# Optimization experiments

Hardware: AMD Instinct MI355X
Metric: run time of the kernel (lower is better)

The kernel has to match this reference:

```python
import jax, jax.numpy as jnp
import numpy as np

N_NODES = 50000
N_EDGES = 800000
DIMS = [100, 512, 256, 128, 200]  # input -> conv1 -> conv2 -> conv3 -> conv4


def setup_inputs() -> dict:
    key = jax.random.key(0)
    ks = jax.random.split(key, 2 + 4)
    x = jax.random.normal(ks[0], (N_NODES, DIMS[0]), dtype=jnp.float32)
    edge_index = jax.random.randint(ks[1], (2, N_EDGES), 0, N_NODES, dtype=jnp.int64)
    inp = {"x": x, "edge_index": edge_index}
    for i in range(4):
        fan_in = DIMS[i]
        W = jax.random.normal(ks[2 + i], (DIMS[i], DIMS[i + 1]), dtype=jnp.float32) * (1.0 / np.sqrt(fan_in)).astype(np.float32)
        b = jnp.zeros((DIMS[i + 1],), dtype=jnp.float32)
        inp[f"W{i + 1}"] = W
        inp[f"b{i + 1}"] = b
    return inp


def _gcn_layer(x, row, col, norm, W, b, n):
    # PyG GCNConv: linear transform first, then normalized scatter-add, then bias.
    h = x @ W                           # [N, out]
    msg = h[row] * norm[:, None]        # [E+N, out] gather + edge scale
    agg = jax.ops.segment_sum(msg, col, num_segments=n)  # scatter-add to targets
    return agg + b


def reference(x, edge_index, W1, b1, W2, b2, W3, b3, W4, b4):
    n = x.shape[0]
    loop = jnp.arange(n, dtype=edge_index.dtype)
    row = jnp.concatenate([edge_index[0], loop])  # sources (with self-loops)
    col = jnp.concatenate([edge_index[1], loop])  # targets (with self-loops)
    deg = jax.ops.segment_sum(jnp.ones_like(col, dtype=x.dtype), col, num_segments=n)
    dinv = jnp.where(deg > 0, jax.lax.rsqrt(deg), 0.0)
    norm = dinv[row] * dinv[col]  # symmetric D^{-1/2}(A+I)D^{-1/2} edge weights

    out = jax.nn.relu(_gcn_layer(x, row, col, norm, W1, b1, n))
    out = jax.nn.relu(_gcn_layer(out, row, col, norm, W2, b2, n))
    out = jax.nn.relu(_gcn_layer(out, row, col, norm, W3, b3, n))
    out = jax.nn.relu(_gcn_layer(out, row, col, norm, W4, b4, n))
    return jnp.mean(out, axis=0, keepdims=True)  # [1, 200]
```

## Files before the change

### kernel.cpp

```cpp
#include <hip/hip_runtime.h>
#include <hip/hip_bf16.h>


#define NN 50000
#define NE 800000
#define NPART 8
#define PRANGE (NN / NPART)

typedef __attribute__((ext_vector_type(8))) _Float16 f16x8;
typedef __attribute__((ext_vector_type(4))) float floatx4;
typedef __attribute__((ext_vector_type(2))) float floatx2;

union U16x8 {
    uint4 u4;
    f16x8 h;
    _Float16 e[8];
};

__device__ __forceinline__ void dec16(const unsigned char* p, float* f) {
    uint4 v = *(const uint4*)p;
    unsigned w[4] = {v.x, v.y, v.z, v.w};
#pragma unroll
    for (int k = 0; k < 4; k++) {
        floatx2 lo = __builtin_amdgcn_cvt_pk_f32_fp8(w[k], false);
        floatx2 hi = __builtin_amdgcn_cvt_pk_f32_fp8(w[k], true);
        f[k * 4 + 0] = lo[0];
        f[k * 4 + 1] = lo[1];
        f[k * 4 + 2] = hi[0];
        f[k * 4 + 3] = hi[1];
    }
}

__device__ __forceinline__ uint4 enc16(const float* f) {
    uint4 r;
    unsigned w;
    w = __builtin_amdgcn_cvt_pk_fp8_f32(f[0], f[1], 0, false);
    w = __builtin_amdgcn_cvt_pk_fp8_f32(f[2], f[3], (int)w, true);
    r.x = w;
    w = __builtin_amdgcn_cvt_pk_fp8_f32(f[4], f[5], 0, false);
    w = __builtin_amdgcn_cvt_pk_fp8_f32(f[6], f[7], (int)w, true);
    r.y = w;
    w = __builtin_amdgcn_cvt_pk_fp8_f32(f[8], f[9], 0, false);
    w = __builtin_amdgcn_cvt_pk_fp8_f32(f[10], f[11], (int)w, true);
    r.z = w;
    w = __builtin_amdgcn_cvt_pk_fp8_f32(f[12], f[13], 0, false);
    w = __builtin_amdgcn_cvt_pk_fp8_f32(f[14], f[15], (int)w, true);
    r.w = w;
    return r;
}

__device__ __forceinline__ uint4 dec8_f16(uint2 v) {
    floatx2 f0 = __builtin_amdgcn_cvt_pk_f32_fp8(v.x, false);
    floatx2 f1 = __builtin_amdgcn_cvt_pk_f32_fp8(v.x, true);
    floatx2 f2 = __builtin_amdgcn_cvt_pk_f32_fp8(v.y, false);
    floatx2 f3 = __builtin_amdgcn_cvt_pk_f32_fp8(v.y, true);
    U16x8 o;
    o.e[0] = (_Float16)f0[0]; o.e[1] = (_Float16)f0[1];
    o.e[2] = (_Float16)f1[0]; o.e[3] = (_Float16)f1[1];
    o.e[4] = (_Float16)f2[0]; o.e[5] = (_Float16)f2[1];
    o.e[6] = (_Float16)f3[0]; o.e[7] = (_Float16)f3[1];
    return o.u4;
}

__global__ __launch_bounds__(256) void zero_detect_kernel(
    const unsigned* __restrict__ ei, int* __restrict__ flag,
    unsigned* __restrict__ cnt, unsigned* __restrict__ fillc,
    float* __restrict__ out) {
    int tid = blockIdx.x * 256 + threadIdx.x;
    if (tid < NN) {
        cnt[tid] = 0u;
        fillc[tid] = 0u;
    }
    if (blockIdx.x == 0) {
        if (threadIdx.x < 200) out[threadIdx.x] = 0.f;
        unsigned w = ei[2 * threadIdx.x + 1];
        unsigned long long any = __ballot(w != 0);
        if (threadIdx.x == 0) *flag = (any == 0ull) ? 1 : 0;
    }
}

__global__ __launch_bounds__(256) void count_kernel(const void* ei,
                                                    const int* __restrict__ flag,
                                                    unsigned* __restrict__ cnt) {
    const int part = blockIdx.x & 7;
    const int lo = part * PRANGE, hi = lo + PRANGE;
    const int group = blockIdx.x >> 3;
    const int f64 = *flag;
    const long long* p64 = (const long long*)ei + NE;
    const int* p32 = (const int*)ei + NE;
    for (int e = group * 256 + threadIdx.x; e < NE; e += 128 * 256) {
        int c = f64 ? (int)p64[e] : p32[e];
        if (c >= lo && c < hi) atomicAdd(&cnt[c], 1u);
    }
}

__global__ __launch_bounds__(256) void scan1_kernel(const unsigned* __restrict__ cnt,
                                                    int* __restrict__ off,
                                                    int* __restrict__ bsum,
                                                    float* __restrict__ dinv) {
    __shared__ int ws[4];
    int b = blockIdx.x, t = threadIdx.x;
    int base = b * 1024 + t * 4;
    int v[4];
    int s = 0;
#pragma unroll
    for (int i = 0; i < 4; i++) {
        int val = 0;
        if (base + i < NN) {
            val = (int)cnt[base + i];
            dinv[base + i] = rsqrtf((float)(val + 1));
        }
        v[i] = s;
        s += val;
    }
    int lane = t & 63, wv = t >> 6;
    int x = s;
    for (int d = 1; d < 64; d <<= 1) {
        int y = __shfl_up(x, d, 64);
        if (lane >= d) x += y;
    }
    if (lane == 63) ws[wv] = x;
    __syncthreads();
    int wpre = 0;
#pragma unroll
    for (int i = 0; i < 4; i++)
        if (i < wv) wpre += ws[i];
    int texcl = x - s + wpre;
#pragma unroll
    for (int i = 0; i < 4; i++)
        if (base + i < NN) off[base + i] = texcl + v[i];
    if (t == 255) bsum[b] = texcl + s;
}

__global__ void scan2_kernel(int* bsum, int nb) {
    int t = threadIdx.x;
    int v = (t < nb) ? bsum[t] : 0;
    int x = v;
    for (int d = 1; d < 64; d <<= 1) {
        int y = __shfl_up(x, d, 64);
        if (t >= d) x += y;
    }
    if (t < nb) bsum[t] = x - v;
}

__global__ __launch_bounds__(256) void scan3_kernel(int* __restrict__ off,
                                                    const int* __restrict__ bsum) {
    int b = blockIdx.x;
    int add = bsum[b];
    int base = b * 1024 + threadIdx.x * 4;
#pragma unroll
    for (int i = 0; i < 4; i++)
        if (base + i < NN) off[base + i] += add;
    if (b == 0 && threadIdx.x == 0) off[NN] = NE;
}

__global__ __launch_bounds__(256) void fill_kernel(
    const void* ei, const int* __restrict__ flag, const int* __restrict__ off,
    unsigned* __restrict__ fillc, int* __restrict__ ep) {
    const int part = blockIdx.x & 7;
    const int lo = part * PRANGE, hi = lo + PRANGE;
    const int group = blockIdx.x >> 3;
    const int f64 = *flag;
    const long long* p64 = (const long long*)ei;
    const int* p32 = (const int*)ei;
    for (int e = group * 256 + threadIdx.x; e < NE; e += 128 * 256) {
        int c = f64 ? (int)p64[NE + e] : p32[NE + e];
        if (c >= lo && c < hi) {
            int r = f64 ? (int)p64[e] : p32[e];
            int pos = off[c] + (int)atomicAdd(&fillc[c], 1u);
            ep[pos] = r;
        }
    }
}

__global__ __launch_bounds__(256) void xwcast_kernel(
    const float* __restrict__ x, unsigned char* __restrict__ xb,
    const float* __restrict__ W1, const float* __restrict__ W2,
    const float* __restrict__ W3, const float* __restrict__ W4,
    _Float16* __restrict__ w1t, _Float16* __restrict__ w2t,
    _Float16* __restrict__ w3t, _Float16* __restrict__ w4t) {
    int bx = blockIdx.x, t = threadIdx.x;
    if (bx < 1563) {
        int tid = bx * 256 + t;
        int node = tid >> 3, sub = tid & 7;
        if (node >= NN) return;
        int base = sub * 16;
        float f[16];
#pragma unroll
        for (int i = 0; i < 16; i++) {
            int c = base + i;
            f[i] = (c < 100) ? x[(size_t)node * 100 + c] : 0.f;
        }
        *(uint4*)(xb + (size_t)node * 128 + base) = enc16(f);
        return;
    }
    int b = bx - 1563;
    const float* W;
    _Float16* Wt;
    int K, N, Kpad, tid;
    if (b < 256)      { W = W1; Wt = w1t; K = 100; N = 512; Kpad = 128; tid = b * 256 + t; }
    else if (b < 768) { W = W2; Wt = w2t; K = 512; N = 256; Kpad = 512; tid = (b - 256) * 256 + t; }
    else if (b < 896) { W = W3; Wt = w3t; K = 256; N = 128; Kpad = 256; tid = (b - 768) * 256 + t; }
    else              { W = W4; Wt = w4t; K = 128; N = 200; Kpad = 128; tid = (b - 896) * 256 + t; }
    int n = tid / Kpad, k = tid - n * Kpad;
    float v = (k < K && n < N) ? W[(size_t)k * N + n] : 0.f;
    Wt[tid] = (_Float16)v;
}

template <int D, int BR>
__global__ __launch_bounds__(256) void agg_kernel(
    const unsigned char* __restrict__ H, const int* __restrict__ off,
    const int* __restrict__ ep, const float* __restrict__ dinv,
    const float* __restrict__ bias, unsigned char* __restrict__ O) {
    constexpr int LPN = D / 16;
    int tid = blockIdx.x * 256 + threadIdx.x;
    int node = tid / LPN;
    int sub = tid % LPN;
    if (node >= NN) return;
    int s = off[node], e = off[node + 1];
    float dc = dinv[node];
    float selfw = dc * dc;
    const int base = sub * 16;
    const unsigned char* __restrict__ Hb = H + base;
    float acc[16], t0[16], t1[16];
    dec16(Hb + (size_t)node * D, t0);
#pragma unroll
    for (int i = 0; i < 16; i++) acc[i] = selfw * t0[i];
    int j = s;
    for (; j + 2 <= e; j += 2) {
        int r0 = ep[j];
        int r1 = ep[j + 1];
        float w0 = dinv[r0] * dc;
        float w1 = dinv[r1] * dc;
        dec16(Hb + (size_t)r0 * D, t0);
        dec16(Hb + (size_t)r1 * D, t1);
#pragma unroll
        for (int i = 0; i < 16; i++) acc[i] = fmaf(w0, t0[i], acc[i]);
#pragma unroll
        for (int i = 0; i < 16; i++) acc[i] = fmaf(w1, t1[i], acc[i]);
    }
    if (j < e) {
        int r0 = ep[j];
        float w0 = dinv[r0] * dc;
        dec16(Hb + (size_t)r0 * D, t0);
#pragma unroll
        for (int i = 0; i < 16; i++) acc[i] = fmaf(w0, t0[i], acc[i]);
    }
    if (BR) {
#pragma unroll
        for (int i = 0; i < 16; i++) acc[i] = fmaxf(acc[i] + bias[base + i], 0.f);
    }
    *(uint4*)(O + (size_t)node * D + base) = enc16(acc);
}

template <int EPI>
__global__ __launch_bounds__(256) void gemm_kernel(
    const unsigned char* __restrict__ A, const _Float16* __restrict__ B,
    const float* __restrict__ bias, unsigned char* __restrict__ Cb,
    float* __restrict__ outmean, int M, int K, int N) {
    __shared__ _Float16 Asl[64 * 36];
    __shared__ _Float16 Bsl[128 * 36];
    __shared__ float red[128];
    const int m0 = blockIdx.y * 64;
    const int n0 = blockIdx.x * 128;
    const int t = threadIdx.x;
    const int lane = t & 63, w = t >> 6;
    const int wm = (w >> 1) * 32, wn = (w & 1) * 64;
    const int r16 = lane & 15, quad = lane >> 4;

    const int arow = t >> 2, ac8 = (t & 3) * 8;
    int gma = m0 + arow; if (gma > M - 1) gma = M - 1;
    const unsigned char* Aptr = A + (size_t)gma * K + ac8;
    const int brow0 = t >> 1, bc8_0 = (t & 1) * 8;
    const int brow1 = 128 + (t >> 1), bc8_1 = bc8_0;
    const int cb0 = t, cb1 = t + 256;
    const int rb0 = cb0 >> 2, kb0 = (cb0 & 3) * 8;
    const int rb1 = cb1 >> 2, kb1 = (cb1 & 3) * 8;
    const _Float16* Bptr0 = B + (size_t)(n0 + rb0) * K + kb0;
    const _Float16* Bptr1 = B + (size_t)(n0 + rb1) * K + kb1;

    floatx4 acc[2][4];
    const floatx4 fz = {0.f, 0.f, 0.f, 0.f};
#pragma unroll
    for (int i = 0; i < 2; i++)
#pragma unroll
        for (int j = 0; j < 4; j++) acc[i][j] = fz;

    uint2 apf = *(const uint2*)Aptr;
    uint4 bpf0 = *(const uint4*)Bptr0;
    uint4 bpf1 = *(const uint4*)Bptr1;

    for (int kc = 0; kc < K; kc += 32) {
        __syncthreads();
        *(uint4*)(Asl + arow * 36 + ac8) = dec8_f16(apf);
        *(uint4*)(Bsl + rb0 * 36 + kb0) = bpf0;
        *(uint4*)(Bsl + rb1 * 36 + kb1) = bpf1;
        __syncthreads();
        if (kc + 32 < K) {
            apf = *(const uint2*)(Aptr + kc + 32);
            bpf0 = *(const uint4*)(Bptr0 + kc + 32);
            bpf1 = *(const uint4*)(Bptr1 + kc + 32);
        }
        f16x8 af[2], bf[4];
#pragma unroll
        for (int i = 0; i < 2; i++)
            af[i] = *(const f16x8*)(Asl + (wm + i * 16 + r16) * 36 + quad * 8);
#pragma unroll
        for (int j = 0; j < 4; j++)
            bf[j] = *(const f16x8*)(Bsl + (wn + j * 16 + r16) * 36 + quad * 8);
#pragma unroll
        for (int i = 0; i < 2; i++)
#pragma unroll
            for (int j = 0; j < 4; j++)
                acc[i][j] = __builtin_amdgcn_mfma_f32_16x16x32_f16(af[i], bf[j], acc[i][j], 0, 0, 0);
    }

    if (EPI == 2) {
        if (t < 128) red[t] = 0.f;
        __syncthreads();
#pragma unroll
        for (int j = 0; j < 4; j++) {
            int col = n0 + wn + j * 16 + r16;
            float s = 0.f;
            if (col < N) {
                float bv = bias[col];
#pragma unroll
                for (int i = 0; i < 2; i++) {
                    int mbase = m0 + wm + i * 16 + quad * 4;
#pragma unroll
                    for (int r = 0; r < 4; r++)
                        if (mbase + r < M) s += fmaxf(acc[i][j][r] + bv, 0.f);
                }
            }
            atomicAdd(&red[wn + j * 16 + r16], s);
        }
        __syncthreads();
        if (t < 128) {
            int col = n0 + t;
            if (col < N) atomicAdd(outmean + col, red[t] * (1.0f / (float)NN));
        }
    } else {
#pragma unroll
        for (int i = 0; i < 2; i++) {
            int mbase = m0 + wm + i * 16 + quad * 4;
#pragma unroll
            for (int r = 0; r < 4; r++) {
                int m = mbase + r;
                if (m >= M) continue;
#pragma unroll
                for (int j = 0; j < 4; j++) {
                    int col = n0 + wn + j * 16 + r16;
                    float v = acc[i][j][r];
                    if (EPI == 1) v = fmaxf(v + bias[col], 0.f);
                    unsigned pk = __builtin_amdgcn_cvt_pk_fp8_f32(v, v, 0, false);
                    Cb[(size_t)m * N + col] = (unsigned char)(pk & 0xffu);
                }
            }
        }
    }
}

extern "C" void kernel_launch(void* const* d_in, const int* in_sizes, int n_in,
                              void* d_out, int out_size, void* d_ws, size_t ws_size,
                              hipStream_t stream) {
    const float* x  = (const float*)d_in[0];
    const void*  ei = d_in[1];
    const float* W1 = (const float*)d_in[2];
    const float* b1 = (const float*)d_in[3];
    const float* W2 = (const float*)d_in[4];
    const float* b2 = (const float*)d_in[5];
    const float* W3 = (const float*)d_in[6];
    const float* b3 = (const float*)d_in[7];
    const float* W4 = (const float*)d_in[8];
    const float* b4 = (const float*)d_in[9];
    float* out = (float*)d_out;

    char* ws = (char*)d_ws;
    size_t o = 0;
    auto alloc = [&](size_t bytes) -> void* {
        void* p = ws + o;
        o += (bytes + 255) & ~(size_t)255;
        return p;
    };
    int*      flag  = (int*)alloc(4);
    unsigned* cnt   = (unsigned*)alloc((size_t)NN * 4);
    int*      off   = (int*)alloc((size_t)(NN + 1) * 4);
    unsigned* fillc = (unsigned*)alloc((size_t)NN * 4);
    float*    dinv  = (float*)alloc((size_t)NN * 4);
    int*      ep    = (int*)alloc((size_t)NE * 4);
    _Float16* w1t = (_Float16*)alloc((size_t)512 * 128 * 2);
    _Float16* w2t = (_Float16*)alloc((size_t)256 * 512 * 2);
    _Float16* w3t = (_Float16*)alloc((size_t)128 * 256 * 2);
    _Float16* w4t = (_Float16*)alloc((size_t)256 * 128 * 2);
    int*      bsum  = (int*)alloc(256);
    unsigned char* xb  = (unsigned char*)alloc((size_t)NN * 128);
    unsigned char* A1b = (unsigned char*)alloc((size_t)NN * 128);
    unsigned char* H1b = (unsigned char*)alloc((size_t)NN * 512);
    unsigned char* t2b = (unsigned char*)alloc((size_t)NN * 256);
    unsigned char* H2b = (unsigned char*)alloc((size_t)NN * 256);
    unsigned char* t3b = (unsigned char*)alloc((size_t)NN * 128);
    unsigned char* h3b = (unsigned char*)alloc((size_t)NN * 128);
    unsigned char* A4b = (unsigned char*)alloc((size_t)NN * 128);

    const int NB1 = (NN + 1023) / 1024;
    const int ZB = (NN + 255) / 256;
    const int PB = 1024;

    zero_detect_kernel<<<ZB, 256, 0, stream>>>((const unsigned*)ei, flag, cnt, fillc, out);
    count_kernel<<<PB, 256, 0, stream>>>(ei, flag, cnt);
    scan1_kernel<<<NB1, 256, 0, stream>>>(cnt, off, bsum, dinv);
    scan2_kernel<<<1, 64, 0, stream>>>(bsum, NB1);
    scan3_kernel<<<NB1, 256, 0, stream>>>(off, bsum);
    fill_kernel<<<PB, 256, 0, stream>>>(ei, flag, off, fillc, ep);
    xwcast_kernel<<<1563 + 1024, 256, 0, stream>>>(x, xb, W1, W2, W3, W4, w1t, w2t, w3t, w4t);

    const int MB64 = (NN + 63) / 64;
    const int AB128 = (NN * 8 + 255) / 256;
    const int AB256 = (NN * 16 + 255) / 256;

    agg_kernel<128, 0><<<AB128, 256, 0, stream>>>(xb, off, ep, dinv, nullptr, A1b);
    gemm_kernel<1><<<dim3(4, MB64), 256, 0, stream>>>(A1b, w1t, b1, H1b, nullptr, NN, 128, 512);
    gemm_kernel<0><<<dim3(2, MB64), 256, 0, stream>>>(H1b, w2t, nullptr, t2b, nullptr, NN, 512, 256);
    agg_kernel<256, 1><<<AB256, 256, 0, stream>>>(t2b, off, ep, dinv, b2, H2b);
    gemm_kernel<0><<<dim3(1, MB64), 256, 0, stream>>>(H2b, w3t, nullptr, t3b, nullptr, NN, 256, 128);
    agg_kernel<128, 1><<<AB128, 256, 0, stream>>>(t3b, off, ep, dinv, b3, h3b);
    agg_kernel<128, 0><<<AB128, 256, 0, stream>>>(h3b, off, ep, dinv, nullptr, A4b);
    gemm_kernel<2><<<dim3(2, MB64), 256, 0, stream>>>(A4b, w4t, b4, nullptr, out, NN, 128, 200);
}
```

Before: 351.1 us.

## Merge all stages into one cooperative persistent kernel with grid syncs

Replaces the sequence of about fifteen separate launches (CSR build, scans, casts, aggregations, GEMMs) with a single cooperative mega-kernel. Each stage becomes a grid-stride or tile-stride phase, and stages are separated by grid.sync(). The grid size comes from an occupancy query capped at 4 blocks per CU times 256. The aim is to remove per-launch overhead and inter-kernel gaps. In exchange, grid-wide barriers are added and occupancy and register use are constrained across all phases, since the GEMM and aggregation code paths now share one kernel's resources.

```diff
diff --git a/kernel.cpp b/kernel.cpp
--- a/kernel.cpp
+++ b/kernel.cpp
@@ -1,11 +1,13 @@
 #include <hip/hip_runtime.h>
 #include <hip/hip_bf16.h>
+#include <hip/hip_cooperative_groups.h>
+
+namespace cg = cooperative_groups;
 
 
 #define NN 50000
 #define NE 800000
-#define NPART 8
-#define PRANGE (NN / NPART)
+#define PRANGE (NN / 8)
 
 typedef __attribute__((ext_vector_type(8))) _Float16 f16x8;
 typedef __attribute__((ext_vector_type(4))) float floatx4;
@@ -62,319 +64,328 @@
     return o.u4;
 }
 
-__global__ __launch_bounds__(256) void zero_detect_kernel(
-    const unsigned* __restrict__ ei, int* __restrict__ flag,
-    unsigned* __restrict__ cnt, unsigned* __restrict__ fillc,
-    float* __restrict__ out) {
-    int tid = blockIdx.x * 256 + threadIdx.x;
-    if (tid < NN) {
-        cnt[tid] = 0u;
-        fillc[tid] = 0u;
-    }
-    if (blockIdx.x == 0) {
-        if (threadIdx.x < 200) out[threadIdx.x] = 0.f;
-        unsigned w = ei[2 * threadIdx.x + 1];
-        unsigned long long any = __ballot(w != 0);
-        if (threadIdx.x == 0) *flag = (any == 0ull) ? 1 : 0;
-    }
-}
-
-__global__ __launch_bounds__(256) void count_kernel(const void* ei,
-                                                    const int* __restrict__ flag,
-                                                    unsigned* __restrict__ cnt) {
-    const int part = blockIdx.x & 7;
-    const int lo = part * PRANGE, hi = lo + PRANGE;
-    const int group = blockIdx.x >> 3;
-    const int f64 = *flag;
-    const long long* p64 = (const long long*)ei + NE;
-    const int* p32 = (const int*)ei + NE;
-    for (int e = group * 256 + threadIdx.x; e < NE; e += 128 * 256) {
-        int c = f64 ? (int)p64[e] : p32[e];
-        if (c >= lo && c < hi) atomicAdd(&cnt[c], 1u);
-    }
-}
-
-__global__ __launch_bounds__(256) void scan1_kernel(const unsigned* __restrict__ cnt,
-                                                    int* __restrict__ off,
-                                                    int* __restrict__ bsum,
-                                                    float* __restrict__ dinv) {
-    __shared__ int ws[4];
-    int b = blockIdx.x, t = threadIdx.x;
-    int base = b * 1024 + t * 4;
-    int v[4];
-    int s = 0;
-#pragma unroll
-    for (int i = 0; i < 4; i++) {
-        int val = 0;
-        if (base + i < NN) {
-            val = (int)cnt[base + i];
-            dinv[base + i] = rsqrtf((float)(val + 1));
-        }
-        v[i] = s;
-        s += val;
-    }
-    int lane = t & 63, wv = t >> 6;
-    int x = s;
-    for (int d = 1; d < 64; d <<= 1) {
-        int y = __shfl_up(x, d, 64);
-        if (lane >= d) x += y;
-    }
-    if (lane == 63) ws[wv] = x;
-    __syncthreads();
-    int wpre = 0;
-#pragma unroll
-    for (int i = 0; i < 4; i++)
-        if (i < wv) wpre += ws[i];
-    int texcl = x - s + wpre;
-#pragma unroll
-    for (int i = 0; i < 4; i++)
-        if (base + i < NN) off[base + i] = texcl + v[i];
-    if (t == 255) bsum[b] = texcl + s;
-}
-
-__global__ void scan2_kernel(int* bsum, int nb) {
-    int t = threadIdx.x;
-    int v = (t < nb) ? bsum[t] : 0;
-    int x = v;
-    for (int d = 1; d < 64; d <<= 1) {
-        int y = __shfl_up(x, d, 64);
-        if (t >= d) x += y;
-    }
-    if (t < nb) bsum[t] = x - v;
-}
-
-__global__ __launch_bounds__(256) void scan3_kernel(int* __restrict__ off,
-                                                    const int* __restrict__ bsum) {
-    int b = blockIdx.x;
-    int add = bsum[b];
-    int base = b * 1024 + threadIdx.x * 4;
-#pragma unroll
-    for (int i = 0; i < 4; i++)
-        if (base + i < NN) off[base + i] += add;
-    if (b == 0 && threadIdx.x == 0) off[NN] = NE;
-}
-
-__global__ __launch_bounds__(256) void fill_kernel(
-    const void* ei, const int* __restrict__ flag, const int* __restrict__ off,
-    unsigned* __restrict__ fillc, int* __restrict__ ep) {
-    const int part = blockIdx.x & 7;
-    const int lo = part * PRANGE, hi = lo + PRANGE;
-    const int group = blockIdx.x >> 3;
-    const int f64 = *flag;
-    const long long* p64 = (const long long*)ei;
-    const int* p32 = (const int*)ei;
-    for (int e = group * 256 + threadIdx.x; e < NE; e += 128 * 256) {
-        int c = f64 ? (int)p64[NE + e] : p32[NE + e];
-        if (c >= lo && c < hi) {
-            int r = f64 ? (int)p64[e] : p32[e];
-            int pos = off[c] + (int)atomicAdd(&fillc[c], 1u);
-            ep[pos] = r;
-        }
-    }
-}
-
-__global__ __launch_bounds__(256) void xwcast_kernel(
-    const float* __restrict__ x, unsigned char* __restrict__ xb,
-    const float* __restrict__ W1, const float* __restrict__ W2,
-    const float* __restrict__ W3, const float* __restrict__ W4,
-    _Float16* __restrict__ w1t, _Float16* __restrict__ w2t,
-    _Float16* __restrict__ w3t, _Float16* __restrict__ w4t) {
-    int bx = blockIdx.x, t = threadIdx.x;
-    if (bx < 1563) {
-        int tid = bx * 256 + t;
-        int node = tid >> 3, sub = tid & 7;
-        if (node >= NN) return;
-        int base = sub * 16;
-        float f[16];
-#pragma unroll
-        for (int i = 0; i < 16; i++) {
-            int c = base + i;
-            f[i] = (c < 100) ? x[(size_t)node * 100 + c] : 0.f;
-        }
-        *(uint4*)(xb + (size_t)node * 128 + base) = enc16(f);
-        return;
-    }
-    int b = bx - 1563;
-    const float* W;
-    _Float16* Wt;
-    int K, N, Kpad, tid;
-    if (b < 256)      { W = W1; Wt = w1t; K = 100; N = 512; Kpad = 128; tid = b * 256 + t; }
-    else if (b < 768) { W = W2; Wt = w2t; K = 512; N = 256; Kpad = 512; tid = (b - 256) * 256 + t; }
-    else if (b < 896) { W = W3; Wt = w3t; K = 256; N = 128; Kpad = 256; tid = (b - 768) * 256 + t; }
-    else              { W = W4; Wt = w4t; K = 128; N = 200; Kpad = 128; tid = (b - 896) * 256 + t; }
-    int n = tid / Kpad, k = tid - n * Kpad;
-    float v = (k < K && n < N) ? W[(size_t)k * N + n] : 0.f;
-    Wt[tid] = (_Float16)v;
-}
+struct MegaParams {
+    const float* x;
+    const void* ei;
+    const float *W1, *b1, *W2, *b2, *W3, *b3, *W4, *b4;
+    float* out;
+    int* flag;
+    unsigned* cnt;
+    int* off;
+    unsigned* fillc;
+    float* dinv;
+    int* ep;
+    int* bsum;
+    _Float16 *w1t, *w2t, *w3t, *w4t;
+    unsigned char *xb, *A1b, *H1b, *t2b, *H2b, *t3b, *h3b, *A4b;
+};
 
 template <int D, int BR>
-__global__ __launch_bounds__(256) void agg_kernel(
+__device__ __forceinline__ void agg_phase(
     const unsigned char* __restrict__ H, const int* __restrict__ off,
     const int* __restrict__ ep, const float* __restrict__ dinv,
-    const float* __restrict__ bias, unsigned char* __restrict__ O) {
+    const float* __restrict__ bias, unsigned char* __restrict__ O,
+    int bid, int nb, int t) {
     constexpr int LPN = D / 16;
-    int tid = blockIdx.x * 256 + threadIdx.x;
-    int node = tid / LPN;
-    int sub = tid % LPN;
-    if (node >= NN) return;
-    int s = off[node], e = off[node + 1];
-    float dc = dinv[node];
-    float selfw = dc * dc;
-    const int base = sub * 16;
-    const unsigned char* __restrict__ Hb = H + base;
-    float acc[16], t0[16], t1[16];
-    dec16(Hb + (size_t)node * D, t0);
-#pragma unroll
-    for (int i = 0; i < 16; i++) acc[i] = selfw * t0[i];
-    int j = s;
-    for (; j + 2 <= e; j += 2) {
-        int r0 = ep[j];
-        int r1 = ep[j + 1];
-        float w0 = dinv[r0] * dc;
-        float w1 = dinv[r1] * dc;
-        dec16(Hb + (size_t)r0 * D, t0);
-        dec16(Hb + (size_t)r1 * D, t1);
-#pragma unroll
-        for (int i = 0; i < 16; i++) acc[i] = fmaf(w0, t0[i], acc[i]);
-#pragma unroll
-        for (int i = 0; i < 16; i++) acc[i] = fmaf(w1, t1[i], acc[i]);
-    }
-    if (j < e) {
-        int r0 = ep[j];
-        float w0 = dinv[r0] * dc;
-        dec16(Hb + (size_t)r0 * D, t0);
-#pragma unroll
-        for (int i = 0; i < 16; i++) acc[i] = fmaf(w0, t0[i], acc[i]);
-    }
-    if (BR) {
-#pragma unroll
-        for (int i = 0; i < 16; i++) acc[i] = fmaxf(acc[i] + bias[base + i], 0.f);
-    }
-    *(uint4*)(O + (size_t)node * D + base) = enc16(acc);
+    const int total = NN * LPN;
+    for (int tid = bid * 256 + t; tid < total; tid += nb * 256) {
+        int node = tid / LPN;
+        int sub = tid % LPN;
+        int s = off[node], e = off[node + 1];
+        float dc = dinv[node];
+        float selfw = dc * dc;
+        const int base = sub * 16;
+        const unsigned char* Hb = H + base;
+        float acc[16], t0[16], t1[16];
+        dec16(Hb + (size_t)node * D, t0);
+#pragma unroll
+        for (int i = 0; i < 16; i++) acc[i] = selfw * t0[i];
+        int j = s;
+        for (; j + 2 <= e; j += 2) {
+            int r0 = ep[j];
+            int r1 = ep[j + 1];
+            float w0 = dinv[r0] * dc;
+            float w1 = dinv[r1] * dc;
+            dec16(Hb + (size_t)r0 * D, t0);
+            dec16(Hb + (size_t)r1 * D, t1);
+#pragma unroll
+            for (int i = 0; i < 16; i++) acc[i] = fmaf(w0, t0[i], acc[i]);
+#pragma unroll
+            for (int i = 0; i < 16; i++) acc[i] = fmaf(w1, t1[i], acc[i]);
+        }
+        if (j < e) {
+            int r0 = ep[j];
+            float w0 = dinv[r0] * dc;
+            dec16(Hb + (size_t)r0 * D, t0);
+#pragma unroll
+            for (int i = 0; i < 16; i++) acc[i] = fmaf(w0, t0[i], acc[i]);
+        }
+        if (BR) {
+#pragma unroll
+            for (int i = 0; i < 16; i++) acc[i] = fmaxf(acc[i] + bias[base + i], 0.f);
+        }
+        *(uint4*)(O + (size_t)node * D + base) = enc16(acc);
+    }
 }
 
 template <int EPI>
-__global__ __launch_bounds__(256) void gemm_kernel(
+__device__ __forceinline__ void gemm_phase(
     const unsigned char* __restrict__ A, const _Float16* __restrict__ B,
     const float* __restrict__ bias, unsigned char* __restrict__ Cb,
-    float* __restrict__ outmean, int M, int K, int N) {
+    float* __restrict__ outmean, int M, int K, int N, int nx,
+    _Float16* Asl, _Float16* Bsl, float* red, int bid, int nb, int t) {
+    const int ny = (M + 63) / 64;
+    const int ntiles = nx * ny;
+    const int lane = t & 63, w = t >> 6;
+    const int wm = (w >> 1) * 32, wn = (w & 1) * 64;
+    const int r16 = lane & 15, quad = lane >> 4;
+    const int arow = t >> 2, ac8 = (t & 3) * 8;
+    const int rb0 = t >> 2, kb0 = (t & 3) * 8;
+    const int rb1 = (t + 256) >> 2, kb1 = kb0;
+
+    for (int tile = bid; tile < ntiles; tile += nb) {
+        const int m0 = (tile / nx) * 64;
+        const int n0 = (tile % nx) * 128;
+        int gma = m0 + arow;
+        if (gma > M - 1) gma = M - 1;
+        const unsigned char* Aptr = A + (size_t)gma * K + ac8;
+        const _Float16* Bptr0 = B + (size_t)(n0 + rb0) * K + kb0;
+        const _Float16* Bptr1 = B + (size_t)(n0 + rb1) * K + kb1;
+
+        floatx4 acc[2][4];
+        const floatx4 fz = {0.f, 0.f, 0.f, 0.f};
+#pragma unroll
+        for (int i = 0; i < 2; i++)
+#pragma unroll
+            for (int j = 0; j < 4; j++) acc[i][j] = fz;
+
+        uint2 apf = *(const uint2*)Aptr;
+        uint4 bpf0 = *(const uint4*)Bptr0;
+        uint4 bpf1 = *(const uint4*)Bptr1;
+
+        for (int kc = 0; kc < K; kc += 32) {
+            __syncthreads();
+            *(uint4*)(Asl + arow * 36 + ac8) = dec8_f16(apf);
+            *(uint4*)(Bsl + rb0 * 36 + kb0) = bpf0;
+            *(uint4*)(Bsl + rb1 * 36 + kb1) = bpf1;
+            __syncthreads();
+            if (kc + 32 < K) {
+                apf = *(const uint2*)(Aptr + kc + 32);
+                bpf0 = *(const uint4*)(Bptr0 + kc + 32);
+                bpf1 = *(const uint4*)(Bptr1 + kc + 32);
+            }
+            f16x8 af[2], bf[4];
+#pragma unroll
+            for (int i = 0; i < 2; i++)
+                af[i] = *(const f16x8*)(Asl + (wm + i * 16 + r16) * 36 + quad * 8);
+#pragma unroll
+            for (int j = 0; j < 4; j++)
+                bf[j] = *(const f16x8*)(Bsl + (wn + j * 16 + r16) * 36 + quad * 8);
+#pragma unroll
+            for (int i = 0; i < 2; i++)
+#pragma unroll
+                for (int j = 0; j < 4; j++)
+                    acc[i][j] = __builtin_amdgcn_mfma_f32_16x16x32_f16(af[i], bf[j], acc[i][j], 0, 0, 0);
+        }
+
+        if (EPI == 2) {
+            if (t < 128) red[t] = 0.f;
+            __syncthreads();
+#pragma unroll
+            for (int j = 0; j < 4; j++) {
+                int col = n0 + wn + j * 16 + r16;
+                float s = 0.f;
+                if (col < N) {
+                    float bv = bias[col];
+#pragma unroll
+                    for (int i = 0; i < 2; i++) {
+                        int mbase = m0 + wm + i * 16 + quad * 4;
+#pragma unroll
+                        for (int r = 0; r < 4; r++)
+                            if (mbase + r < M) s += fmaxf(acc[i][j][r] + bv, 0.f);
+                    }
+                }
+                atomicAdd(&red[wn + j * 16 + r16], s);
+            }
+            __syncthreads();
+            if (t < 128) {
+                int col = n0 + t;
+                if (col < N) atomicAdd(outmean + col, red[t] * (1.0f / (float)NN));
+            }
+            __syncthreads();
+        } else {
+#pragma unroll
+            for (int i = 0; i < 2; i++) {
+                int mbase = m0 + wm + i * 16 + quad * 4;
+#pragma unroll
+                for (int r = 0; r < 4; r++) {
+                    int m = mbase + r;
+                    if (m >= M) continue;
+#pragma unroll
+                    for (int j = 0; j < 4; j++) {
+                        int col = n0 + wn + j * 16 + r16;
+                        float v = acc[i][j][r];
+                        if (EPI == 1) v = fmaxf(v + bias[col], 0.f);
+                        unsigned pk = __builtin_amdgcn_cvt_pk_fp8_f32(v, v, 0, false);
+                        Cb[(size_t)m * N + col] = (unsigned char)(pk & 0xffu);
+                    }
+                }
+            }
+        }
+    }
+}
+
+__global__ __launch_bounds__(256, 3) void mega_kernel(MegaParams p) {
+    cg::grid_group grid = cg::this_grid();
+    const int bid = blockIdx.x, nb = gridDim.x, t = threadIdx.x;
     __shared__ _Float16 Asl[64 * 36];
     __shared__ _Float16 Bsl[128 * 36];
     __shared__ float red[128];
-    const int m0 = blockIdx.y * 64;
-    const int n0 = blockIdx.x * 128;
-    const int t = threadIdx.x;
-    const int lane = t & 63, w = t >> 6;
-    const int wm = (w >> 1) * 32, wn = (w & 1) * 64;
-    const int r16 = lane & 15, quad = lane >> 4;
-
-    const int arow = t >> 2, ac8 = (t & 3) * 8;
-    int gma = m0 + arow; if (gma > M - 1) gma = M - 1;
-    const unsigned char* Aptr = A + (size_t)gma * K + ac8;
-    const int brow0 = t >> 1, bc8_0 = (t & 1) * 8;
-    const int brow1 = 128 + (t >> 1), bc8_1 = bc8_0;
-    const int cb0 = t, cb1 = t + 256;
-    const int rb0 = cb0 >> 2, kb0 = (cb0 & 3) * 8;
-    const int rb1 = cb1 >> 2, kb1 = (cb1 & 3) * 8;
-    const _Float16* Bptr0 = B + (size_t)(n0 + rb0) * K + kb0;
-    const _Float16* Bptr1 = B + (size_t)(n0 + rb1) * K + kb1;
-
-    floatx4 acc[2][4];
-    const floatx4 fz = {0.f, 0.f, 0.f, 0.f};
-#pragma unroll
-    for (int i = 0; i < 2; i++)
-#pragma unroll
-        for (int j = 0; j < 4; j++) acc[i][j] = fz;
-
-    uint2 apf = *(const uint2*)Aptr;
-    uint4 bpf0 = *(const uint4*)Bptr0;
-    uint4 bpf1 = *(const uint4*)Bptr1;
-
-    for (int kc = 0; kc < K; kc += 32) {
+    __shared__ int sws[4];
+
+    for (int i = bid * 256 + t; i < NN; i += nb * 256) {
+        p.cnt[i] = 0u;
+        p.fillc[i] = 0u;
+    }
+    if (bid == 0) {
+        if (t < 200) p.out[t] = 0.f;
+        unsigned w = ((const unsigned*)p.ei)[2 * t + 1];
+        unsigned long long any = __ballot(w != 0);
+        if (t == 0) *p.flag = (any == 0ull) ? 1 : 0;
+    }
+    grid.sync();
+
+    const int f64 = *(volatile const int*)p.flag;
+
+    {
+        const int part = bid & 7;
+        const int lo = part * PRANGE, hi = lo + PRANGE;
+        const int group = bid >> 3, ngroup = nb >> 3;
+        const long long* q64 = (const long long*)p.ei + NE;
+        const int* q32 = (const int*)p.ei + NE;
+        for (int e = group * 256 + t; e < NE; e += ngroup * 256) {
+            int c = f64 ? (int)q64[e] : q32[e];
+            if (c >= lo && c < hi) atomicAdd(&p.cnt[c], 1u);
+        }
+        for (int idx = bid * 256 + t; idx < NN * 8; idx += nb * 256) {
+            int node = idx >> 3, sub = idx & 7;
+            int base = sub * 16;
+            float f[16];
+#pragma unroll
+            for (int i = 0; i < 16; i++) {
+                int c = base + i;
+                f[i] = (c < 100) ? p.x[(size_t)node * 100 + c] : 0.f;
+            }
+            *(uint4*)(p.xb + (size_t)node * 128 + base) = enc16(f);
+        }
+        for (int vb = bid; vb < 1024; vb += nb) {
+            const float* W;
+            _Float16* Wt;
+            int K, N, Kpad, tid;
+            if (vb < 256)      { W = p.W1; Wt = p.w1t; K = 100; N = 512; Kpad = 128; tid = vb * 256 + t; }
+            else if (vb < 768) { W = p.W2; Wt = p.w2t; K = 512; N = 256; Kpad = 512; tid = (vb - 256) * 256 + t; }
+            else if (vb < 896) { W = p.W3; Wt = p.w3t; K = 256; N = 128; Kpad = 256; tid = (vb - 768) * 256 + t; }
+            else               { W = p.W4; Wt = p.w4t; K = 128; N = 200; Kpad = 128; tid = (vb - 896) * 256 + t; }
+            int n = tid / Kpad, k = tid - n * Kpad;
+            float v = (k < K && n < N) ? W[(size_t)k * N + n] : 0.f;
+            Wt[tid] = (_Float16)v;
+        }
+    }
+    grid.sync();
+
+    for (int vb = bid; vb < 49; vb += nb) {
+        int base = vb * 1024 + t * 4;
+        int v[4];
+        int s = 0;
+#pragma unroll
+        for (int i = 0; i < 4; i++) {
+            int val = 0;
+            if (base + i < NN) {
+                val = (int)p.cnt[base + i];
+                p.dinv[base + i] = rsqrtf((float)(val + 1));
+            }
+            v[i] = s;
+            s += val;
+        }
+        int lane = t & 63, wv = t >> 6;
+        int xx = s;
+        for (int d = 1; d < 64; d <<= 1) {
+            int y = __shfl_up(xx, d, 64);
+            if (lane >= d) xx += y;
+        }
+        if (lane == 63) sws[wv] = xx;
         __syncthreads();
-        *(uint4*)(Asl + arow * 36 + ac8) = dec8_f16(apf);
-        *(uint4*)(Bsl + rb0 * 36 + kb0) = bpf0;
-        *(uint4*)(Bsl + rb1 * 36 + kb1) = bpf1;
+        int wpre = 0;
+#pragma unroll
+        for (int i = 0; i < 4; i++)
+            if (i < wv) wpre += sws[i];
+        int texcl = xx - s + wpre;
+#pragma unroll
+        for (int i = 0; i < 4; i++)
+            if (base + i < NN) p.off[base + i] = texcl + v[i];
+        if (t == 255) p.bsum[vb] = texcl + s;
         __syncthreads();
-        if (kc + 32 < K) {
-            apf = *(const uint2*)(Aptr + kc + 32);
-            bpf0 = *(const uint4*)(Bptr0 + kc + 32);
-            bpf1 = *(const uint4*)(Bptr1 + kc + 32);
-        }
-        f16x8 af[2], bf[4];
-#pragma unroll
-        for (int i = 0; i < 2; i++)
-            af[i] = *(const f16x8*)(Asl + (wm + i * 16 + r16) * 36 + quad * 8);
-#pragma unroll
-        for (int j = 0; j < 4; j++)
-            bf[j] = *(const f16x8*)(Bsl + (wn + j * 16 + r16) * 36 + quad * 8);
-#pragma unroll
-        for (int i = 0; i < 2; i++)
-#pragma unroll
-            for (int j = 0; j < 4; j++)
-                acc[i][j] = __builtin_amdgcn_mfma_f32_16x16x32_f16(af[i], bf[j], acc[i][j], 0, 0, 0);
-    }
-
-    if (EPI == 2) {
-        if (t < 128) red[t] = 0.f;
-        __syncthreads();
-#pragma unroll
-        for (int j = 0; j < 4; j++) {
-            int col = n0 + wn + j * 16 + r16;
-            float s = 0.f;
-            if (col < N) {
-                float bv = bias[col];
-#pragma unroll
-                for (int i = 0; i < 2; i++) {
-                    int mbase = m0 + wm + i * 16 + quad * 4;
-#pragma unroll
-                    for (int r = 0; r < 4; r++)
-                        if (mbase + r < M) s += fmaxf(acc[i][j][r] + bv, 0.f);
-                }
-            }
-            atomicAdd(&red[wn + j * 16 + r16], s);
-        }
-        __syncthreads();
-        if (t < 128) {
-            int col = n0 + t;
-            if (col < N) atomicAdd(outmean + col, red[t] * (1.0f / (float)NN));
-        }
-    } else {
-#pragma unroll
-        for (int i = 0; i < 2; i++) {
-            int mbase = m0 + wm + i * 16 + quad * 4;
-#pragma unroll
-            for (int r = 0; r < 4; r++) {
-                int m = mbase + r;
-                if (m >= M) continue;
-#pragma unroll
-                for (int j = 0; j < 4; j++) {
-                    int col = n0 + wn + j * 16 + r16;
-                    float v = acc[i][j][r];
-                    if (EPI == 1) v = fmaxf(v + bias[col], 0.f);
-                    unsigned pk = __builtin_amdgcn_cvt_pk_fp8_f32(v, v, 0, false);
-                    Cb[(size_t)m * N + col] = (unsigned char)(pk & 0xffu);
-                }
-            }
-        }
-    }
+    }
+    grid.sync();
+
+    if (bid == 0 && t < 64) {
+        int v = (t < 49) ? p.bsum[t] : 0;
+        int xx = v;
+        for (int d = 1; d < 64; d <<= 1) {
+            int y = __shfl_up(xx, d, 64);
+            if (t >= d) xx += y;
+        }
+        if (t < 49) p.bsum[t] = xx - v;
+    }
+    grid.sync();
+
+    for (int vb = bid; vb < 49; vb += nb) {
+        int add = p.bsum[vb];
+        int base = vb * 1024 + t * 4;
+#pragma unroll
+        for (int i = 0; i < 4; i++)
+            if (base + i < NN) p.off[base + i] += add;
+    }
+    if (bid == 0 && t == 0) p.off[NN] = NE;
+    grid.sync();
+
+    {
+        const int part = bid & 7;
+        const int lo = part * PRANGE, hi = lo + PRANGE;
+        const int group = bid >> 3, ngroup = nb >> 3;
+        const long long* q64 = (const long long*)p.ei;
+        const int* q32 = (const int*)p.ei;
+        for (int e = group * 256 + t; e < NE; e += ngroup * 256) {
+            int c = f64 ? (int)q64[NE + e] : q32[NE + e];
+            if (c >= lo && c < hi) {
+                int r = f64 ? (int)q64[e] : q32[e];
+                int pos = p.off[c] + (int)atomicAdd(&p.fillc[c], 1u);
+                p.ep[pos] = r;
+            }
+        }
+    }
+    grid.sync();
+
+    agg_phase<128, 0>(p.xb, p.off, p.ep, p.dinv, nullptr, p.A1b, bid, nb, t);
+    grid.sync();
+    gemm_phase<1>(p.A1b, p.w1t, p.b1, p.H1b, nullptr, NN, 128, 512, 4, Asl, Bsl, red, bid, nb, t);
+    grid.sync();
+    gemm_phase<0>(p.H1b, p.w2t, nullptr, p.t2b, nullptr, NN, 512, 256, 2, Asl, Bsl, red, bid, nb, t);
+    grid.sync();
+    agg_phase<256, 1>(p.t2b, p.off, p.ep, p.dinv, p.b2, p.H2b, bid, nb, t);
+    grid.sync();
+    gemm_phase<0>(p.H2b, p.w3t, nullptr, p.t3b, nullptr, NN, 256, 128, 1, Asl, Bsl, red, bid, nb, t);
+    grid.sync();
+    agg_phase<128, 1>(p.t3b, p.off, p.ep, p.dinv, p.b3, p.h3b, bid, nb, t);
+    grid.sync();
+    agg_phase<128, 0>(p.h3b, p.off, p.ep, p.dinv, nullptr, p.A4b, bid, nb, t);
+    grid.sync();
+    gemm_phase<2>(p.A4b, p.w4t, p.b4, nullptr, p.out, NN, 128, 200, 2, Asl, Bsl, red, bid, nb, t);
 }
 
 extern "C" void kernel_launch(void* const* d_in, const int* in_sizes, int n_in,
                               void* d_out, int out_size, void* d_ws, size_t ws_size,
                               hipStream_t stream) {
-    const float* x  = (const float*)d_in[0];
-    const void*  ei = d_in[1];
-    const float* W1 = (const float*)d_in[2];
-    const float* b1 = (const float*)d_in[3];
-    const float* W2 = (const float*)d_in[4];
-    const float* b2 = (const float*)d_in[5];
-    const float* W3 = (const float*)d_in[6];
-    const float* b3 = (const float*)d_in[7];
-    const float* W4 = (const float*)d_in[8];
-    const float* b4 = (const float*)d_in[9];
-    float* out = (float*)d_out;
-
     char* ws = (char*)d_ws;
     size_t o = 0;
     auto alloc = [&](size_t bytes) -> void* {
@@ -382,48 +393,46 @@
         o += (bytes + 255) & ~(size_t)255;
         return p;
     };
-    int*      flag  = (int*)alloc(4);
-    unsigned* cnt   = (unsigned*)alloc((size_t)NN * 4);
-    int*      off   = (int*)alloc((size_t)(NN + 1) * 4);
-    unsigned* fillc = (unsigned*)alloc((size_t)NN * 4);
-    float*    dinv  = (float*)alloc((size_t)NN * 4);
-    int*      ep    = (int*)alloc((size_t)NE * 4);
-    _Float16* w1t = (_Float16*)alloc((size_t)512 * 128 * 2);
-    _Float16* w2t = (_Float16*)alloc((size_t)256 * 512 * 2);
-    _Float16* w3t = (_Float16*)alloc((size_t)128 * 256 * 2);
-    _Float16* w4t = (_Float16*)alloc((size_t)256 * 128 * 2);
-    int*      bsum  = (int*)alloc(256);
-    unsigned char* xb  = (unsigned char*)alloc((size_t)NN * 128);
-    unsigned char* A1b = (unsigned char*)alloc((size_t)NN * 128);
-    unsigned char* H1b = (unsigned char*)alloc((size_t)NN * 512);
-    unsigned char* t2b = (unsigned char*)alloc((size_t)NN * 256);
-    unsigned char* H2b = (unsigned char*)alloc((size_t)NN * 256);
-    unsigned char* t3b = (unsigned char*)alloc((size_t)NN * 128);
-    unsigned char* h3b = (unsigned char*)alloc((size_t)NN * 128);
-    unsigned char* A4b = (unsigned char*)alloc((size_t)NN * 128);
-
-    const int NB1 = (NN + 1023) / 1024;
-    const int ZB = (NN + 255) / 256;
-    const int PB = 1024;
-
-    zero_detect_kernel<<<ZB, 256, 0, stream>>>((const unsigned*)ei, flag, cnt, fillc, out);
-    count_kernel<<<PB, 256, 0, stream>>>(ei, flag, cnt);
-    scan1_kernel<<<NB1, 256, 0, stream>>>(cnt, off, bsum, dinv);
-    scan2_kernel<<<1, 64, 0, stream>>>(bsum, NB1);
-    scan3_kernel<<<NB1, 256, 0, stream>>>(off, bsum);
-    fill_kernel<<<PB, 256, 0, stream>>>(ei, flag, off, fillc, ep);
-    xwcast_kernel<<<1563 + 1024, 256, 0, stream>>>(x, xb, W1, W2, W3, W4, w1t, w2t, w3t, w4t);
-
-    const int MB64 = (NN + 63) / 64;
-    const int AB128 = (NN * 8 + 255) / 256;
-    const int AB256 = (NN * 16 + 255) / 256;
-
-    agg_kernel<128, 0><<<AB128, 256, 0, stream>>>(xb, off, ep, dinv, nullptr, A1b);
-    gemm_kernel<1><<<dim3(4, MB64), 256, 0, stream>>>(A1b, w1t, b1, H1b, nullptr, NN, 128, 512);
-    gemm_kernel<0><<<dim3(2, MB64), 256, 0, stream>>>(H1b, w2t, nullptr, t2b, nullptr, NN, 512, 256);
-    agg_kernel<256, 1><<<AB256, 256, 0, stream>>>(t2b, off, ep, dinv, b2, H2b);
-    gemm_kernel<0><<<dim3(1, MB64), 256, 0, stream>>>(H2b, w3t, nullptr, t3b, nullptr, NN, 256, 128);
-    agg_kernel<128, 1><<<AB128, 256, 0, stream>>>(t3b, off, ep, dinv, b3, h3b);
-    agg_kernel<128, 0><<<AB128, 256, 0, stream>>>(h3b, off, ep, dinv, nullptr, A4b);
-    gemm_kernel<2><<<dim3(2, MB64), 256, 0, stream>>>(A4b, w4t, b4, nullptr, out, NN, 128, 200);
-}
+
+    MegaParams p;
+    p.x  = (const float*)d_in[0];
+    p.ei = d_in[1];
+    p.W1 = (const float*)d_in[2];
+    p.b1 = (const float*)d_in[3];
+    p.W2 = (const float*)d_in[4];
+    p.b2 = (const float*)d_in[5];
+    p.W3 = (const float*)d_in[6];
+    p.b3 = (const float*)d_in[7];
+    p.W4 = (const float*)d_in[8];
+    p.b4 = (const float*)d_in[9];
+    p.out = (float*)d_out;
+
+    p.flag  = (int*)alloc(4);
+    p.cnt   = (unsigned*)alloc((size_t)NN * 4);
+    p.off   = (int*)alloc((size_t)(NN + 1) * 4);
+    p.fillc = (unsigned*)alloc((size_t)NN * 4);
+    p.dinv  = (float*)alloc((size_t)NN * 4);
+    p.ep    = (int*)alloc((size_t)NE * 4);
+    p.bsum  = (int*)alloc(256);
+    p.w1t = (_Float16*)alloc((size_t)512 * 128 * 2);
+    p.w2t = (_Float16*)alloc((size_t)256 * 512 * 2);
+    p.w3t = (_Float16*)alloc((size_t)128 * 256 * 2);
+    p.w4t = (_Float16*)alloc((size_t)256 * 128 * 2);
+    p.xb  = (unsigned char*)alloc((size_t)NN * 128);
+    p.A1b = (unsigned char*)alloc((size_t)NN * 128);
+    p.H1b = (unsigned char*)alloc((size_t)NN * 512);
+    p.t2b = (unsigned char*)alloc((size_t)NN * 256);
+    p.H2b = (unsigned char*)alloc((size_t)NN * 256);
+    p.t3b = (unsigned char*)alloc((size_t)NN * 128);
+    p.h3b = (unsigned char*)alloc((size_t)NN * 128);
+    p.A4b = (unsigned char*)alloc((size_t)NN * 128);
+
+    int occ = 0;
+    if (hipOccupancyMaxActiveBlocksPerMultiprocessor(&occ, mega_kernel, 256, 0) != hipSuccess || occ < 1)
+        occ = 2;
+    if (occ > 4) occ = 4;
+    int nblk = occ * 256;
+
+    void* args[] = {&p};
+    hipLaunchCooperativeKernel((void*)mega_kernel, dim3(nblk), dim3(256), args, 0, stream);
+}
```

After: 1.331 ms. 279% more time.
